# Optimization experiments

Measured on AMD Instinct MI355X. Metric: run time of the kernel, lower is better.

Reference implementation:

```python
import jax, jax.numpy as jnp
import numpy as np

N_NODES = 100000
N_EDGES = 1600000
FEAT = 128
HID = 128
CLS = 4


def setup_inputs() -> dict:
    key = jax.random.key(0)
    ks = jax.random.split(key, 10)
    x = jax.random.normal(ks[0], (N_NODES, FEAT), dtype=jnp.float32)
    edge_index = jax.random.randint(ks[1], (2, N_EDGES), 0, N_NODES, dtype=jnp.int64)
    s1 = 1.0 / np.sqrt(FEAT)
    s2 = 1.0 / np.sqrt(HID)
    s3 = 1.0 / np.sqrt(CLS)
    return {
        "x": x,
        "edge_index": edge_index,
        "W1l": jax.random.uniform(ks[2], (HID, FEAT), jnp.float32, -s1, s1),
        "b1": jax.random.uniform(ks[3], (HID,), jnp.float32, -s1, s1),
        "W1r": jax.random.uniform(ks[4], (HID, FEAT), jnp.float32, -s1, s1),
        "W2l": jax.random.uniform(ks[5], (CLS, HID), jnp.float32, -s2, s2),
        "b2": jax.random.uniform(ks[6], (CLS,), jnp.float32, -s2, s2),
        "W2r": jax.random.uniform(ks[7], (CLS, HID), jnp.float32, -s2, s2),
        "Wlin": jax.random.uniform(ks[8], (2, CLS), jnp.float32, -s3, s3),
        "blin": jax.random.uniform(ks[9], (2,), jnp.float32, -s3, s3),
    }


def _sage_conv(h, src, dst, Wl, bl, Wr, n_nodes):
    # PyG SAGEConv (mean aggr, root_weight=True): lin_l(mean_j h_j) + lin_r(h_i)
    msg = h[src]  # [E, d] irregular gather
    agg = jax.ops.segment_sum(msg, dst, num_segments=n_nodes)  # [N, d]
    deg = jax.ops.segment_sum(jnp.ones((src.shape[0], 1), h.dtype), dst,
                              num_segments=n_nodes)  # [N, 1]
    agg = agg / jnp.maximum(deg, 1.0)
    return agg @ Wl.T + bl + h @ Wr.T


def reference(x, edge_index, W1l, b1, W1r, W2l, b2, W2r, Wlin, blin):
    n = x.shape[0]
    src, dst = edge_index[0], edge_index[1]
    h = jax.nn.relu(_sage_conv(x, src, dst, W1l, b1, W1r, n))
    # dropout is identity in eval mode (training=False)
    h = _sage_conv(h, src, dst, W2l, b2, W2r, n)  # [N, 4]
    return h @ Wlin.T + blin  # [N, 2]
```

## Files before the change

### kernel.cpp

```cpp
#include <hip/hip_runtime.h>

#define NN 100000
#define NE 1600000
#define NBUK 1563
#define EB 8192

typedef __attribute__((ext_vector_type(8))) short v8s;
typedef __attribute__((ext_vector_type(4))) float v4f;

__device__ __forceinline__ unsigned short f2bf(float f) {
  unsigned int u = __float_as_uint(f);
  unsigned int r = (u + 0x7FFFu + ((u >> 16) & 1u)) >> 16;
  return (unsigned short)r;
}
__device__ __forceinline__ float bflo(unsigned int w) { return __uint_as_float(w << 16); }
__device__ __forceinline__ float bfhi(unsigned int w) { return __uint_as_float(w & 0xFFFF0000u); }
__device__ __forceinline__ float bf2f(unsigned short w) {
  return __uint_as_float((unsigned int)w << 16);
}


__global__ void k_zerob(int* __restrict__ hist) {
  int i = blockIdx.x * blockDim.x + threadIdx.x;
  if (i < NBUK) hist[i] = 0;
}

__global__ __launch_bounds__(256) void k_hist(const int* __restrict__ dst,
                                              int* __restrict__ hist) {
  __shared__ int lh[NBUK];
  int t = threadIdx.x;
  for (int i = t; i < NBUK; i += 256) lh[i] = 0;
  __syncthreads();
  int base = blockIdx.x * 16384;
  int lim = min(16384, NE - base);
  for (int j = t; j < lim; j += 256) atomicAdd(&lh[dst[base + j] >> 6], 1);
  __syncthreads();
  for (int i = t; i < NBUK; i += 256) {
    int c = lh[i];
    if (c) atomicAdd(&hist[i], c);
  }
}

__global__ __launch_bounds__(256) void k_scanb(const int* __restrict__ hist,
                                               int* __restrict__ bbase,
                                               int* __restrict__ gcur) {
  __shared__ int sc[256];
  __shared__ int carry;
  int t = threadIdx.x;
  if (t == 0) carry = 0;
  __syncthreads();
  for (int c = 0; c < (NBUK + 255) / 256; ++c) {
    int i = c * 256 + t;
    int vv = (i < NBUK) ? hist[i] : 0;
    sc[t] = vv;
    __syncthreads();
    for (int o = 1; o < 256; o <<= 1) {
      int uu = (t >= o) ? sc[t - o] : 0;
      __syncthreads();
      sc[t] += uu;
      __syncthreads();
    }
    int excl = carry + sc[t] - vv;
    if (i < NBUK) { bbase[i] = excl; gcur[i] = excl; }
    __syncthreads();
    if (t == 0) carry += sc[255];
    __syncthreads();
  }
}

extern __shared__ char smem_dyn[];
__global__ __launch_bounds__(256) void k_scatter(const int* __restrict__ src,
                                                 const int* __restrict__ dst,
                                                 int* __restrict__ gcur,
                                                 unsigned int* __restrict__ staged) {
  unsigned int* stageP = (unsigned int*)smem_dyn;
  unsigned short* stageB = (unsigned short*)(stageP + EB);
  int* lhist  = (int*)(stageB + EB);
  int* lbase  = lhist + NBUK;
  int* lcur   = lbase + NBUK;
  int* gclaim = lcur + NBUK;
  __shared__ int sc[256];
  __shared__ int carry;
  int t = threadIdx.x;
  int e0 = blockIdx.x * EB;
  int ecnt = min(EB, NE - e0);
  for (int i = t; i < NBUK; i += 256) lhist[i] = 0;
  if (t == 0) carry = 0;
  __syncthreads();
  for (int j = t; j < ecnt; j += 256) atomicAdd(&lhist[dst[e0 + j] >> 6], 1);
  __syncthreads();
  for (int c = 0; c < (NBUK + 255) / 256; ++c) {
    int i = c * 256 + t;
    int vv = (i < NBUK) ? lhist[i] : 0;
    sc[t] = vv;
    __syncthreads();
    for (int o = 1; o < 256; o <<= 1) {
      int uu = (t >= o) ? sc[t - o] : 0;
      __syncthreads();
      sc[t] += uu;
      __syncthreads();
    }
    int excl = carry + sc[t] - vv;
    if (i < NBUK) { lbase[i] = excl; lcur[i] = excl; }
    __syncthreads();
    if (t == 0) carry += sc[255];
    __syncthreads();
  }
  for (int b = t; b < NBUK; b += 256) {
    int c = lhist[b];
    gclaim[b] = c ? atomicAdd(&gcur[b], c) : 0;
  }
  __syncthreads();
  for (int j = t; j < ecnt; j += 256) {
    int s = src[e0 + j], d = dst[e0 + j];
    int b = d >> 6;
    int lp = atomicAdd(&lcur[b], 1);
    stageP[lp] = ((unsigned int)s << 6) | (unsigned int)(d & 63);
    stageB[lp] = (unsigned short)b;
  }
  __syncthreads();
  for (int i = t; i < ecnt; i += 256) {
    int b = stageB[i];
    staged[gclaim[b] + (i - lbase[b])] = stageP[i];
  }
}

__global__ __launch_bounds__(256) void k_sort2(const unsigned int* __restrict__ staged,
                                               const int* __restrict__ bbase,
                                               const int* __restrict__ hist,
                                               int* __restrict__ csr,
                                               int* __restrict__ off,
                                               int* __restrict__ deg) {
  __shared__ int h64[64], c64[64];
  int bkt = blockIdx.x, t = threadIdx.x;
  if (t < 64) h64[t] = 0;
  __syncthreads();
  int st = bbase[bkt], cnt = hist[bkt];
  for (int j = t; j < cnt; j += 256) atomicAdd(&h64[staged[st + j] & 63], 1);
  __syncthreads();
  if (t < 64) {
    int v = h64[t];
    int inc = v;
    for (int o = 1; o < 64; o <<= 1) {
      int uu = __shfl_up(inc, o, 64);
      if (t >= o) inc += uu;
    }
    int excl = inc - v;
    c64[t] = excl;
    int node = bkt * 64 + t;
    if (node < NN) { off[node] = st + excl; deg[node] = v; }
  }
  __syncthreads();
  for (int j = t; j < cnt; j += 256) {
    unsigned pk = staged[st + j];
    int lp = atomicAdd(&c64[pk & 63], 1);
    csr[st + lp] = (int)(pk >> 6);
  }
}


__global__ void k_packw(const float* __restrict__ W1l, const float* __restrict__ W1r,
                        unsigned short* __restrict__ Wcat) {
  int i = blockIdx.x * blockDim.x + threadIdx.x;
  float f = (i < 16384) ? W1l[i] : W1r[i - 16384];
  Wcat[i] = f2bf(f);
}

__global__ __launch_bounds__(256) void k_gemm1(
    const float* __restrict__ x, const unsigned short* __restrict__ Wcat,
    unsigned short* __restrict__ u, unsigned short* __restrict__ v) {
  char* wlds = smem_dyn;
  int t = threadIdx.x;
  {
    int rsub = t >> 4, chunk = t & 15;
#pragma unroll
    for (int rd = 0; rd < 16; ++rd) {
      int row = rd * 16 + rsub;
      uint4 w4 = *(const uint4*)(Wcat + (size_t)row * 128 + chunk * 8);
      *(uint4*)(wlds + row * 272 + chunk * 16) = w4;
    }
  }

  int wave = t >> 6, l = t & 63;
  int m0 = blockIdx.x * 64 + wave * 16;
  int lr = l & 15, kq = l >> 4;
  int rowc = min(m0 + lr, NN - 1);

  v8s a[4];
#pragma unroll
  for (int ks = 0; ks < 4; ++ks) {
    const float* xp = x + (size_t)rowc * 128 + ks * 32 + kq * 8;
    float4 f0 = *(const float4*)xp;
    float4 f1 = *(const float4*)(xp + 4);
    v8s tv;
    tv[0] = (short)f2bf(f0.x); tv[1] = (short)f2bf(f0.y);
    tv[2] = (short)f2bf(f0.z); tv[3] = (short)f2bf(f0.w);
    tv[4] = (short)f2bf(f1.x); tv[5] = (short)f2bf(f1.y);
    tv[6] = (short)f2bf(f1.z); tv[7] = (short)f2bf(f1.w);
    a[ks] = tv;
  }

  __syncthreads();

  v4f acc[16];
#pragma unroll
  for (int nt = 0; nt < 16; ++nt) acc[nt] = (v4f){0.f, 0.f, 0.f, 0.f};

#pragma unroll
  for (int nt = 0; nt < 16; ++nt) {
    const char* wrow = wlds + (nt * 16 + lr) * 272;
#pragma unroll
    for (int ks = 0; ks < 4; ++ks) {
      v8s b = *(const v8s*)(wrow + ks * 64 + kq * 16);
      acc[nt] = __builtin_amdgcn_mfma_f32_16x16x32_bf16(b, a[ks], acc[nt], 0, 0, 0);
    }
  }

  if (m0 + lr < NN) {
    size_t rowb = (size_t)(m0 + lr) * 128;
#pragma unroll
    for (int nt = 0; nt < 16; ++nt) {
      unsigned lo = (unsigned)f2bf(acc[nt][0]) | ((unsigned)f2bf(acc[nt][1]) << 16);
      unsigned hi = (unsigned)f2bf(acc[nt][2]) | ((unsigned)f2bf(acc[nt][3]) << 16);
      int col = (nt & 7) * 16 + kq * 4;
      if (nt < 8) *(uint2*)(u + rowb + col) = make_uint2(lo, hi);
      else        *(uint2*)(v + rowb + col) = make_uint2(lo, hi);
    }
  }
}

__global__ __launch_bounds__(256) void k_agg(
    const unsigned short* __restrict__ u, const unsigned short* __restrict__ v,
    const int* __restrict__ csr, const int* __restrict__ off, const int* __restrict__ deg,
    const float* __restrict__ b1,
    const float* __restrict__ W2l, const float* __restrict__ W2r,
    float* __restrict__ p, float* __restrict__ r) {
  int wid = (blockIdx.x * blockDim.x + threadIdx.x) >> 6;
  int l = threadIdx.x & 63;
  if (wid >= NN) return;
  int cnt = deg[wid], st = off[wid];
  int half = l >> 5;
  int dpos = l & 31;
  const char* ubase = (const char*)u + (dpos << 3);

  uint2 vw = *(const uint2*)((const char*)v + ((size_t)wid << 8) + (dpos << 3));
  float4 bb = *(const float4*)(b1 + 4 * dpos);
  const float* Wbase = half ? W2r : W2l;
  float4 wv[4];
#pragma unroll
  for (int o = 0; o < 4; ++o) wv[o] = *(const float4*)(Wbase + o * 128 + 4 * dpos);

  float a0 = 0.f, a1 = 0.f, a2 = 0.f, a3 = 0.f;

#define LOADW(W, S) uint2 W = *(const uint2*)(ubase + ((size_t)((unsigned)(S) << 8)))
#define ACCW(W) { a0 += bflo(W.x); a1 += bfhi(W.x); a2 += bflo(W.y); a3 += bfhi(W.y); }

  for (int base = 0; base < cnt; base += 64) {
    int nloc = min(64, cnt - base);
    int idx = 0;
    if (l < nloc) idx = csr[st + base + l];
    int npair = nloc >> 1;
    int e = 0;
    for (; e + 8 <= npair; e += 8) {
      int s0 = __shfl(idx, 2 * e + half, 64);
      int s1 = __shfl(idx, 2 * (e + 1) + half, 64);
      int s2 = __shfl(idx, 2 * (e + 2) + half, 64);
      int s3 = __shfl(idx, 2 * (e + 3) + half, 64);
      int s4 = __shfl(idx, 2 * (e + 4) + half, 64);
      int s5 = __shfl(idx, 2 * (e + 5) + half, 64);
      int s6 = __shfl(idx, 2 * (e + 6) + half, 64);
      int s7 = __shfl(idx, 2 * (e + 7) + half, 64);
      LOADW(w0, s0);
      LOADW(w1, s1);
      LOADW(w2, s2);
      LOADW(w3, s3);
      LOADW(w4, s4);
      LOADW(w5, s5);
      LOADW(w6, s6);
      LOADW(w7, s7);
      ACCW(w0); ACCW(w1); ACCW(w2); ACCW(w3);
      ACCW(w4); ACCW(w5); ACCW(w6); ACCW(w7);
    }
    for (; e + 4 <= npair; e += 4) {
      int s0 = __shfl(idx, 2 * e + half, 64);
      int s1 = __shfl(idx, 2 * (e + 1) + half, 64);
      int s2 = __shfl(idx, 2 * (e + 2) + half, 64);
      int s3 = __shfl(idx, 2 * (e + 3) + half, 64);
      LOADW(w0, s0);
      LOADW(w1, s1);
      LOADW(w2, s2);
      LOADW(w3, s3);
      ACCW(w0); ACCW(w1); ACCW(w2); ACCW(w3);
    }
    for (; e < npair; ++e) {
      int s = __shfl(idx, 2 * e + half, 64);
      LOADW(w, s);
      ACCW(w);
    }
    if (nloc & 1) {
      int s = __shfl(idx, nloc - 1, 64);
      if (half == 0) {
        LOADW(w, s);
        ACCW(w);
      }
    }
  }
#undef LOADW
#undef ACCW

  a0 += __shfl_xor(a0, 32, 64);
  a1 += __shfl_xor(a1, 32, 64);
  a2 += __shfl_xor(a2, 32, 64);
  a3 += __shfl_xor(a3, 32, 64);

  float inv = 1.f / (float)max(cnt, 1);
  float h0 = fmaxf(fmaf(a0, inv, bflo(vw.x) + bb.x), 0.f);
  float h1 = fmaxf(fmaf(a1, inv, bfhi(vw.x) + bb.y), 0.f);
  float h2 = fmaxf(fmaf(a2, inv, bflo(vw.y) + bb.z), 0.f);
  float h3 = fmaxf(fmaf(a3, inv, bfhi(vw.y) + bb.w), 0.f);

  float t0 = h0 * wv[0].x + h1 * wv[0].y + h2 * wv[0].z + h3 * wv[0].w;
  float t1 = h0 * wv[1].x + h1 * wv[1].y + h2 * wv[1].z + h3 * wv[1].w;
  float t2 = h0 * wv[2].x + h1 * wv[2].y + h2 * wv[2].z + h3 * wv[2].w;
  float t3 = h0 * wv[3].x + h1 * wv[3].y + h2 * wv[3].z + h3 * wv[3].w;
  float v01 = (l & 1) ? t1 : t0;
  float w01 = __shfl_xor((l & 1) ? t0 : t1, 1, 64);
  float r01 = v01 + w01;
  float v23 = (l & 1) ? t3 : t2;
  float w23 = __shfl_xor((l & 1) ? t2 : t3, 1, 64);
  float r23 = v23 + w23;
  float vq = (l & 2) ? r23 : r01;
  float wq = __shfl_xor((l & 2) ? r01 : r23, 2, 64);
  float rr = vq + wq;
  rr += __shfl_xor(rr, 4, 64);
  rr += __shfl_xor(rr, 8, 64);
  rr += __shfl_xor(rr, 16, 64);
  float* outp = half ? r : p;
  if (dpos < 4) outp[(size_t)wid * 4 + dpos] = rr;
}

__global__ __launch_bounds__(256) void k_final(
    const float* __restrict__ p, const float* __restrict__ r,
    const int* __restrict__ csr, const int* __restrict__ off,
    const int* __restrict__ deg,
    const float* __restrict__ b2,
    const float* __restrict__ Wlin, const float* __restrict__ blin,
    float* __restrict__ out) {
  int gid = blockIdx.x * blockDim.x + threadIdx.x;
  int node = gid >> 3;
  int sl = gid & 7;
  if (node >= NN) return;
  int cnt = deg[node], st = off[node];
  int l = threadIdx.x & 63;

  float a0 = 0.f, a1 = 0.f, a2 = 0.f, a3 = 0.f;
  for (int e = sl; e < cnt; e += 8) {
    int s = csr[st + e];
    const float4 pv = *(const float4*)(p + (size_t)s * 4);
    a0 += pv.x; a1 += pv.y; a2 += pv.z; a3 += pv.w;
  }
  float v01 = (l & 1) ? a1 : a0;
  float w01 = __shfl_xor((l & 1) ? a0 : a1, 1, 64);
  float r01 = v01 + w01;
  float v23 = (l & 1) ? a3 : a2;
  float w23 = __shfl_xor((l & 1) ? a2 : a3, 1, 64);
  float r23 = v23 + w23;
  float vq = (l & 2) ? r23 : r01;
  float wq = __shfl_xor((l & 2) ? r01 : r23, 2, 64);
  float rr = vq + wq;
  rr += __shfl_xor(rr, 4, 64);
  int o = sl & 3;
  float inv = 1.f / (float)max(cnt, 1);
  float g = rr * inv + b2[o] + r[(size_t)node * 4 + o];
  float t0 = g * Wlin[o];
  float t1 = g * Wlin[4 + o];
  float vv = (l & 1) ? t1 : t0;
  float ww = __shfl_xor((l & 1) ? t0 : t1, 1, 64);
  float q = vv + ww;
  q += __shfl_xor(q, 2, 64);
  if (sl < 2) out[(size_t)node * 2 + sl] = q + blin[sl];
}


extern "C" void kernel_launch(void* const* d_in, const int* in_sizes, int n_in,
                              void* d_out, int out_size, void* d_ws, size_t ws_size,
                              hipStream_t stream) {
  const float* x    = (const float*)d_in[0];
  const int*   ei   = (const int*)d_in[1];
  const int*   src  = ei;
  const int*   dst  = ei + NE;
  const float* W1l  = (const float*)d_in[2];
  const float* b1   = (const float*)d_in[3];
  const float* W1r  = (const float*)d_in[4];
  const float* W2l  = (const float*)d_in[5];
  const float* b2   = (const float*)d_in[6];
  const float* W2r  = (const float*)d_in[7];
  const float* Wlin = (const float*)d_in[8];
  const float* blin = (const float*)d_in[9];
  float* out = (float*)d_out;

  char* w = (char*)d_ws;
  size_t o = 0;
  auto alloc = [&](size_t bytes) {
    void* pp = (void*)(w + o);
    o = (o + bytes + 255) & ~(size_t)255;
    return pp;
  };
  int* hist  = (int*)alloc(NBUK * 4);
  int* bbase = (int*)alloc(NBUK * 4);
  int* gcur  = (int*)alloc(NBUK * 4);
  unsigned int*  staged = (unsigned int*)alloc((size_t)NE * 4);
  int* csr   = (int*)alloc((size_t)NE * 4);
  int* offs  = (int*)alloc(NN * 4);
  int* deg   = (int*)alloc(NN * 4);
  unsigned short* Wcat  = (unsigned short*)alloc(256 * 128 * 2);
  unsigned short* ubuf  = (unsigned short*)alloc((size_t)NN * 128 * 2);
  unsigned short* vbuf  = (unsigned short*)alloc((size_t)NN * 128 * 2);
  float* pbuf = (float*)alloc((size_t)NN * 4 * 4);
  float* rbuf = (float*)alloc((size_t)NN * 4 * 4);

  const size_t scatter_lds = (size_t)EB * 4 + (size_t)EB * 2 + (size_t)4 * NBUK * 4;
  const size_t gemm1_lds = 256 * 272;

  hipLaunchKernelGGL(k_zerob, dim3((NBUK + 255) / 256), dim3(256), 0, stream, hist);
  hipLaunchKernelGGL(k_hist,  dim3((NE + 16383) / 16384), dim3(256), 0, stream, dst, hist);
  hipLaunchKernelGGL(k_scanb, dim3(1), dim3(256), 0, stream, hist, bbase, gcur);
  hipLaunchKernelGGL(k_scatter, dim3((NE + EB - 1) / EB), dim3(256), scatter_lds, stream,
                     src, dst, gcur, staged);
  hipLaunchKernelGGL(k_sort2, dim3(NBUK), dim3(256), 0, stream,
                     staged, bbase, hist, csr, offs, deg);
  hipLaunchKernelGGL(k_packw, dim3(128), dim3(256), 0, stream, W1l, W1r, Wcat);
  hipLaunchKernelGGL(k_gemm1, dim3((NN + 63) / 64), dim3(256), gemm1_lds, stream,
                     x, Wcat, ubuf, vbuf);
  hipLaunchKernelGGL(k_agg,   dim3((NN * 64 + 255) / 256), dim3(256), 0, stream,
                     ubuf, vbuf, csr, offs, deg, b1, W2l, W2r, pbuf, rbuf);
  hipLaunchKernelGGL(k_final, dim3((NN * 8 + 255) / 256), dim3(256), 0, stream,
                     pbuf, rbuf, csr, offs, deg, b2, Wlin, blin, out);
}
```

Measured before the change: 281.0 us.

## Streamline CSR build: wave-shuffle scan, drop scatter staging, fuse weight packing into GEMM

Replaces the LDS-barrier prefix scans with wave shuffle scans in k_scanb and removes the per-block scan and LDS staging in k_scatter, so edges are written straight to their claimed global slots. It also shrinks the histogram work per block to launch more blocks, folds the bf16 weight packing into k_gemm1 so one launch disappears, and doubles the GEMM block to 512 threads covering 128 rows. The aim is fewer barriers and launches and better parallelism in preprocessing. The trade-off is that scatter writes within a bucket become non-coalesced and order-nondeterministic, and every GEMM block now converts the fp32 weights itself.

```diff
diff --git a/kernel.cpp b/kernel.cpp
--- a/kernel.cpp
+++ b/kernel.cpp
@@ -31,8 +31,8 @@
   int t = threadIdx.x;
   for (int i = t; i < NBUK; i += 256) lh[i] = 0;
   __syncthreads();
-  int base = blockIdx.x * 16384;
-  int lim = min(16384, NE - base);
+  int base = blockIdx.x * 4096;
+  int lim = min(4096, NE - base);
   for (int j = t; j < lim; j += 256) atomicAdd(&lh[dst[base + j] >> 6], 1);
   __syncthreads();
   for (int i = t; i < NBUK; i += 256) {
@@ -44,68 +44,44 @@
 __global__ __launch_bounds__(256) void k_scanb(const int* __restrict__ hist,
                                                int* __restrict__ bbase,
                                                int* __restrict__ gcur) {
-  __shared__ int sc[256];
-  __shared__ int carry;
-  int t = threadIdx.x;
-  if (t == 0) carry = 0;
-  __syncthreads();
+  __shared__ int wsum[4];
+  int t = threadIdx.x, w = t >> 6, l = t & 63;
+  int carry = 0;
   for (int c = 0; c < (NBUK + 255) / 256; ++c) {
     int i = c * 256 + t;
     int vv = (i < NBUK) ? hist[i] : 0;
-    sc[t] = vv;
+    int inc = vv;
+#pragma unroll
+    for (int o = 1; o < 64; o <<= 1) {
+      int uu = __shfl_up(inc, o, 64);
+      if (l >= o) inc += uu;
+    }
+    if (l == 63) wsum[w] = inc;
     __syncthreads();
-    for (int o = 1; o < 256; o <<= 1) {
-      int uu = (t >= o) ? sc[t - o] : 0;
-      __syncthreads();
-      sc[t] += uu;
-      __syncthreads();
-    }
-    int excl = carry + sc[t] - vv;
+    int woff = 0;
+    for (int j = 0; j < w; ++j) woff += wsum[j];
+    int excl = carry + woff + inc - vv;
     if (i < NBUK) { bbase[i] = excl; gcur[i] = excl; }
+    int tot = wsum[0] + wsum[1] + wsum[2] + wsum[3];
     __syncthreads();
-    if (t == 0) carry += sc[255];
-    __syncthreads();
-  }
-}
-
-extern __shared__ char smem_dyn[];
+    carry += tot;
+  }
+}
+
 __global__ __launch_bounds__(256) void k_scatter(const int* __restrict__ src,
                                                  const int* __restrict__ dst,
                                                  int* __restrict__ gcur,
                                                  unsigned int* __restrict__ staged) {
-  unsigned int* stageP = (unsigned int*)smem_dyn;
-  unsigned short* stageB = (unsigned short*)(stageP + EB);
-  int* lhist  = (int*)(stageB + EB);
-  int* lbase  = lhist + NBUK;
-  int* lcur   = lbase + NBUK;
-  int* gclaim = lcur + NBUK;
-  __shared__ int sc[256];
-  __shared__ int carry;
+  __shared__ int lhist[NBUK];
+  __shared__ int lcur[NBUK];
+  __shared__ int gclaim[NBUK];
   int t = threadIdx.x;
   int e0 = blockIdx.x * EB;
   int ecnt = min(EB, NE - e0);
-  for (int i = t; i < NBUK; i += 256) lhist[i] = 0;
-  if (t == 0) carry = 0;
+  for (int i = t; i < NBUK; i += 256) { lhist[i] = 0; lcur[i] = 0; }
   __syncthreads();
   for (int j = t; j < ecnt; j += 256) atomicAdd(&lhist[dst[e0 + j] >> 6], 1);
   __syncthreads();
-  for (int c = 0; c < (NBUK + 255) / 256; ++c) {
-    int i = c * 256 + t;
-    int vv = (i < NBUK) ? lhist[i] : 0;
-    sc[t] = vv;
-    __syncthreads();
-    for (int o = 1; o < 256; o <<= 1) {
-      int uu = (t >= o) ? sc[t - o] : 0;
-      __syncthreads();
-      sc[t] += uu;
-      __syncthreads();
-    }
-    int excl = carry + sc[t] - vv;
-    if (i < NBUK) { lbase[i] = excl; lcur[i] = excl; }
-    __syncthreads();
-    if (t == 0) carry += sc[255];
-    __syncthreads();
-  }
   for (int b = t; b < NBUK; b += 256) {
     int c = lhist[b];
     gclaim[b] = c ? atomicAdd(&gcur[b], c) : 0;
@@ -115,13 +91,7 @@
     int s = src[e0 + j], d = dst[e0 + j];
     int b = d >> 6;
     int lp = atomicAdd(&lcur[b], 1);
-    stageP[lp] = ((unsigned int)s << 6) | (unsigned int)(d & 63);
-    stageB[lp] = (unsigned short)b;
-  }
-  __syncthreads();
-  for (int i = t; i < ecnt; i += 256) {
-    int b = stageB[i];
-    staged[gclaim[b] + (i - lbase[b])] = stageP[i];
+    staged[gclaim[b] + lp] = ((unsigned int)s << 6) | (unsigned int)(d & 63);
   }
 }
 
@@ -158,31 +128,32 @@
   }
 }
 
-
-__global__ void k_packw(const float* __restrict__ W1l, const float* __restrict__ W1r,
-                        unsigned short* __restrict__ Wcat) {
-  int i = blockIdx.x * blockDim.x + threadIdx.x;
-  float f = (i < 16384) ? W1l[i] : W1r[i - 16384];
-  Wcat[i] = f2bf(f);
-}
-
-__global__ __launch_bounds__(256) void k_gemm1(
-    const float* __restrict__ x, const unsigned short* __restrict__ Wcat,
+extern __shared__ char smem_dyn[];
+__global__ __launch_bounds__(512) void k_gemm1(
+    const float* __restrict__ x, const float* __restrict__ W1l,
+    const float* __restrict__ W1r,
     unsigned short* __restrict__ u, unsigned short* __restrict__ v) {
   char* wlds = smem_dyn;
   int t = threadIdx.x;
   {
     int rsub = t >> 4, chunk = t & 15;
 #pragma unroll
-    for (int rd = 0; rd < 16; ++rd) {
-      int row = rd * 16 + rsub;
-      uint4 w4 = *(const uint4*)(Wcat + (size_t)row * 128 + chunk * 8);
-      *(uint4*)(wlds + row * 272 + chunk * 16) = w4;
+    for (int rd = 0; rd < 8; ++rd) {
+      int row = rd * 32 + rsub;
+      const float* wsrc = (row < 128) ? (W1l + (size_t)row * 128 + chunk * 8)
+                                      : (W1r + (size_t)(row - 128) * 128 + chunk * 8);
+      float4 f0 = *(const float4*)wsrc;
+      float4 f1 = *(const float4*)(wsrc + 4);
+      unsigned d0 = (unsigned)f2bf(f0.x) | ((unsigned)f2bf(f0.y) << 16);
+      unsigned d1 = (unsigned)f2bf(f0.z) | ((unsigned)f2bf(f0.w) << 16);
+      unsigned d2 = (unsigned)f2bf(f1.x) | ((unsigned)f2bf(f1.y) << 16);
+      unsigned d3 = (unsigned)f2bf(f1.z) | ((unsigned)f2bf(f1.w) << 16);
+      *(uint4*)(wlds + row * 272 + chunk * 16) = make_uint4(d0, d1, d2, d3);
     }
   }
 
   int wave = t >> 6, l = t & 63;
-  int m0 = blockIdx.x * 64 + wave * 16;
+  int m0 = blockIdx.x * 128 + wave * 16;
   int lr = l & 15, kq = l >> 4;
   int rowc = min(m0 + lr, NN - 1);
 
@@ -413,25 +384,22 @@
   int* csr   = (int*)alloc((size_t)NE * 4);
   int* offs  = (int*)alloc(NN * 4);
   int* deg   = (int*)alloc(NN * 4);
-  unsigned short* Wcat  = (unsigned short*)alloc(256 * 128 * 2);
   unsigned short* ubuf  = (unsigned short*)alloc((size_t)NN * 128 * 2);
   unsigned short* vbuf  = (unsigned short*)alloc((size_t)NN * 128 * 2);
   float* pbuf = (float*)alloc((size_t)NN * 4 * 4);
   float* rbuf = (float*)alloc((size_t)NN * 4 * 4);
 
-  const size_t scatter_lds = (size_t)EB * 4 + (size_t)EB * 2 + (size_t)4 * NBUK * 4;
   const size_t gemm1_lds = 256 * 272;
 
   hipLaunchKernelGGL(k_zerob, dim3((NBUK + 255) / 256), dim3(256), 0, stream, hist);
-  hipLaunchKernelGGL(k_hist,  dim3((NE + 16383) / 16384), dim3(256), 0, stream, dst, hist);
+  hipLaunchKernelGGL(k_hist,  dim3((NE + 4095) / 4096), dim3(256), 0, stream, dst, hist);
   hipLaunchKernelGGL(k_scanb, dim3(1), dim3(256), 0, stream, hist, bbase, gcur);
-  hipLaunchKernelGGL(k_scatter, dim3((NE + EB - 1) / EB), dim3(256), scatter_lds, stream,
+  hipLaunchKernelGGL(k_scatter, dim3((NE + EB - 1) / EB), dim3(256), 0, stream,
                      src, dst, gcur, staged);
   hipLaunchKernelGGL(k_sort2, dim3(NBUK), dim3(256), 0, stream,
                      staged, bbase, hist, csr, offs, deg);
-  hipLaunchKernelGGL(k_packw, dim3(128), dim3(256), 0, stream, W1l, W1r, Wcat);
-  hipLaunchKernelGGL(k_gemm1, dim3((NN + 63) / 64), dim3(256), gemm1_lds, stream,
-                     x, Wcat, ubuf, vbuf);
+  hipLaunchKernelGGL(k_gemm1, dim3((NN + 127) / 128), dim3(512), gemm1_lds, stream,
+                     x, W1l, W1r, ubuf, vbuf);
   hipLaunchKernelGGL(k_agg,   dim3((NN * 64 + 255) / 256), dim3(256), 0, stream,
                      ubuf, vbuf, csr, offs, deg, b1, W2l, W2r, pbuf, rbuf);
   hipLaunchKernelGGL(k_final, dim3((NN * 8 + 255) / 256), dim3(256), 0, stream,
```

Result: faster. 269.2 us (-4.2%).
